# Kernel optimization log

Hardware: AMD Instinct MI355X
Metric: run time of the kernel (lower is better)

## Reference

```python
import jax, jax.numpy as jnp
import numpy as np

DIM = 1024
HEADS = 16
HEAD_DIM = DIM // HEADS
SCALE = HEAD_DIM ** -0.5
B, N = 2, 2048


def setup_inputs() -> dict:
    key = jax.random.key(0)
    ks = jax.random.split(key, 12)
    s = DIM ** -0.5
    return {
        "x_real": jax.random.normal(ks[0], (B, N, DIM), jnp.float32),
        "x_imag": jax.random.normal(ks[1], (B, N, DIM), jnp.float32),
        "Wqkv_r": jax.random.normal(ks[2], (3 * DIM, DIM), jnp.float32) * s,
        "bqkv_r": jax.random.normal(ks[3], (3 * DIM,), jnp.float32) * 0.01,
        "Wqkv_i": jax.random.normal(ks[4], (3 * DIM, DIM), jnp.float32) * s,
        "bqkv_i": jax.random.normal(ks[5], (3 * DIM,), jnp.float32) * 0.01,
        "Wout_r": jax.random.normal(ks[6], (DIM, DIM), jnp.float32) * s,
        "bout_r": jax.random.normal(ks[7], (DIM,), jnp.float32) * 0.01,
        "Wout_i": jax.random.normal(ks[8], (DIM, DIM), jnp.float32) * s,
        "bout_i": jax.random.normal(ks[9], (DIM,), jnp.float32) * 0.01,
    }


def _split_heads(qkv):
    # (B, N, 3*D) -> q, k, v each (B, H, N, hd)
    b, n, _ = qkv.shape
    qkv = qkv.reshape(b, n, 3, HEADS, HEAD_DIM).transpose(2, 0, 3, 1, 4)
    return qkv[0], qkv[1], qkv[2]


def reference(x_real, x_imag, Wqkv_r, bqkv_r, Wqkv_i, bqkv_i,
              Wout_r, bout_r, Wout_i, bout_i):
    b, n, d = x_real.shape
    q_r, k_r, v_r = _split_heads(x_real @ Wqkv_r.T + bqkv_r)
    q_i, k_i, v_i = _split_heads(x_imag @ Wqkv_i.T + bqkv_i)

    # complex score: (q_r + i q_i) (k_r - i k_i)^T pattern per source
    attn_real = (jnp.einsum('bhqd,bhkd->bhqk', q_r, k_r)
                 + jnp.einsum('bhqd,bhkd->bhqk', q_i, k_i)) * SCALE
    attn_imag = (jnp.einsum('bhqd,bhkd->bhqk', q_i, k_r)
                 - jnp.einsum('bhqd,bhkd->bhqk', q_r, k_i)) * SCALE
    attn_mag = jnp.sqrt(attn_real ** 2 + attn_imag ** 2)
    w = jax.nn.softmax(attn_mag, axis=-1)

    out_r = jnp.einsum('bhqk,bhkd->bhqd', w, v_r).transpose(0, 2, 1, 3).reshape(b, n, d)
    out_i = jnp.einsum('bhqk,bhkd->bhqd', w, v_i).transpose(0, 2, 1, 3).reshape(b, n, d)
    out_r = out_r @ Wout_r.T + bout_r
    out_i = out_i @ Wout_i.T + bout_i
    return out_r, out_i
```

## Files before the change

kernel.cpp:

```cpp
#include <hip/hip_runtime.h>


#define DIM_   1024
#define HEADS_ 16
#define HD_    64
#define BB_    2
#define NN_    2048
#define MTOT_  (BB_*NN_)
#define SCALE_ 0.125f
#define QSCALE_ 0.1803368801111243f

typedef __bf16 bf16;
typedef __bf16 bf16x8 __attribute__((ext_vector_type(8)));
typedef short  s16x8  __attribute__((ext_vector_type(8)));
typedef float  fx4    __attribute__((ext_vector_type(4)));

__device__ __forceinline__ bf16x8 neg8(bf16x8 v) {
    s16x8 s;
    __builtin_memcpy(&s, &v, sizeof(s));
    s ^= (short)0x8000;
    bf16x8 r;
    __builtin_memcpy(&r, &s, sizeof(r));
    return r;
}

__device__ __forceinline__ void gl_lds16(const void* g, void* l) {
    __builtin_amdgcn_global_load_lds(
        (const __attribute__((address_space(1))) unsigned int*)g,
        (__attribute__((address_space(3))) unsigned int*)l, 16, 0, 0);
}

#define PIPE_SYNC() asm volatile("s_waitcnt vmcnt(2)\n\ts_barrier" ::: "memory")
#define FULL_SYNC() asm volatile("s_waitcnt vmcnt(0)\n\ts_barrier" ::: "memory")

__global__ __launch_bounds__(256) void cvt_prepass(
    const float* __restrict__ xr, const float* __restrict__ xi,
    const float* __restrict__ wqr, const float* __restrict__ wqi,
    const float* __restrict__ wor, const float* __restrict__ woi,
    bf16* __restrict__ xbf, bf16* __restrict__ wqkv, bf16* __restrict__ wout)
{
    const int bid = blockIdx.x;
    const float* src; bf16* dst; int rel;
    if      (bid < 2048) { src = xr;  dst = xbf;           rel = bid; }
    else if (bid < 4096) { src = xi;  dst = xbf + 4194304; rel = bid - 2048; }
    else if (bid < 5632) { src = wqr; dst = wqkv;          rel = bid - 4096; }
    else if (bid < 7168) { src = wqi; dst = wqkv + 3145728; rel = bid - 5632; }
    else if (bid < 7680) { src = wor; dst = wout;          rel = bid - 7168; }
    else                 { src = woi; dst = wout + 1048576; rel = bid - 7680; }
    size_t base = (size_t)rel * 2048 + (size_t)threadIdx.x * 8;
    fx4 a = *(const fx4*)(src + base);
    fx4 b = *(const fx4*)(src + base + 4);
    bf16x8 o;
#pragma unroll
    for (int j = 0; j < 4; ++j) { o[j] = (bf16)a[j]; o[j+4] = (bf16)b[j]; }
    *(bf16x8*)(dst + base) = o;
}

#define GEMM_CORE(Aptr, Bptr)                                                  \
    __shared__ __align__(16) bf16 As[128*64];                                  \
    __shared__ __align__(16) bf16 Bs[128*64];                                  \
    const int tid  = threadIdx.x;                                              \
    const int w    = tid >> 6, lane = tid & 63;                                \
    const int quad = lane >> 4, lc = lane & 15;                                \
    const int wm   = (w >> 1) * 64, wn = (w & 1) * 64;                         \
    const int rj   = lane >> 3;                                                \
    const int sc   = (lane & 7) ^ rj;                                          \
    const fx4 fzero = {0.f, 0.f, 0.f, 0.f};                                    \
    fx4 acc[4][4];                                                             \
    _Pragma("unroll")                                                          \
    for (int mi = 0; mi < 4; ++mi)                                             \
        _Pragma("unroll")                                                      \
        for (int ni = 0; ni < 4; ++ni) acc[mi][ni] = fzero;                    \
    for (int k0 = 0; k0 < DIM_; k0 += 64) {                                    \
        _Pragma("unroll")                                                      \
        for (int j = 0; j < 4; ++j) {                                          \
            int grp = j*4 + w;                                                 \
            int gr  = grp*8 + rj;                                              \
            gl_lds16(Aptr + (size_t)(m0+gr)*DIM_ + k0 + sc*8, As + grp*512);   \
            gl_lds16(Bptr + (size_t)(n0+gr)*DIM_ + k0 + sc*8, Bs + grp*512);   \
        }                                                                      \
        __syncthreads();                                                       \
        bf16x8 af[2][4], bfr[2][4];                                            \
        _Pragma("unroll")                                                      \
        for (int ks = 0; ks < 2; ++ks) {                                       \
            _Pragma("unroll")                                                  \
            for (int mi = 0; mi < 4; ++mi)                                     \
                af[ks][mi] = *(bf16x8*)&As[(wm+mi*16+lc)*64 + (((ks*4+quad)^(lc&7))*8)]; \
            _Pragma("unroll")                                                  \
            for (int ni = 0; ni < 4; ++ni)                                     \
                bfr[ks][ni] = *(bf16x8*)&Bs[(wn+ni*16+lc)*64 + (((ks*4+quad)^(lc&7))*8)]; \
        }                                                                      \
        _Pragma("unroll")                                                      \
        for (int ks = 0; ks < 2; ++ks)                                         \
            _Pragma("unroll")                                                  \
            for (int mi = 0; mi < 4; ++mi)                                     \
                _Pragma("unroll")                                              \
                for (int ni = 0; ni < 4; ++ni)                                 \
                    acc[mi][ni] = __builtin_amdgcn_mfma_f32_16x16x32_bf16(     \
                        af[ks][mi], bfr[ks][ni], acc[mi][ni], 0, 0, 0);        \
        __syncthreads();                                                       \
    }

__global__ __launch_bounds__(256) void qkv_gemm_dma(
    const bf16* __restrict__ xbf, const bf16* __restrict__ wqkv,
    const float* __restrict__ br, const float* __restrict__ bi,
    bf16* __restrict__ qbuf, bf16* __restrict__ kbuf, bf16* __restrict__ vbuf)
{
    const int z = blockIdx.z;
    const bf16* __restrict__ Ap = xbf  + (size_t)z * 4194304;
    const bf16* __restrict__ Bp = wqkv + (size_t)z * 3145728;
    const float* __restrict__ bias = z ? bi : br;
    const int n0 = blockIdx.x * 128;
    const int m0 = blockIdx.y * 128;

    GEMM_CORE(Ap, Bp)

#pragma unroll
    for (int mi = 0; mi < 4; ++mi)
#pragma unroll
        for (int ni = 0; ni < 4; ++ni)
#pragma unroll
            for (int r = 0; r < 4; ++r) {
                int gm = m0 + wm + mi*16 + quad*4 + r;
                int gc = n0 + wn + ni*16 + lc;
                float val = acc[mi][ni][r] + bias[gc];
                int which = gc >> 10, h = (gc >> 6) & 15, hd = gc & 63;
                if (which == 0) val *= QSCALE_;
                bf16 bv = (bf16)val;
                int b = gm >> 11, n = gm & 2047;
                size_t base = (size_t)((z*BB_ + b)*HEADS_ + h);
                if (which == 0)      qbuf[(base*NN_ + n)*HD_ + hd] = bv;
                else if (which == 1) kbuf[(base*NN_ + n)*HD_ + hd] = bv;
                else                 vbuf[(base*HD_ + hd)*NN_ + n] = bv;
            }
}

__global__ __launch_bounds__(256) void out_gemm_dma(
    const bf16* __restrict__ obuf, const bf16* __restrict__ wout,
    const float* __restrict__ br, const float* __restrict__ bi,
    float* __restrict__ out)
{
    const int z = blockIdx.z;
    const bf16* __restrict__ Ap = obuf + (size_t)z * 4194304;
    const bf16* __restrict__ Bp = wout + (size_t)z * 1048576;
    const float* __restrict__ bias = z ? bi : br;
    float* __restrict__ dst = out + (size_t)z * 4194304;
    const int n0 = blockIdx.x * 128;
    const int m0 = blockIdx.y * 128;

    GEMM_CORE(Ap, Bp)

#pragma unroll
    for (int mi = 0; mi < 4; ++mi)
#pragma unroll
        for (int ni = 0; ni < 4; ++ni)
#pragma unroll
            for (int r = 0; r < 4; ++r) {
                int gm = m0 + wm + mi*16 + quad*4 + r;
                int gc = n0 + wn + ni*16 + lc;
                dst[(size_t)gm*DIM_ + gc] = acc[mi][ni][r] + bias[gc];
            }
}

#define KT 32
#define NSTEP (NN_/KT)

__global__ __launch_bounds__(512, 4) void attn_fwd(
    const bf16* __restrict__ qbuf, const bf16* __restrict__ kbuf,
    const bf16* __restrict__ vbuf, bf16* __restrict__ obuf)
{
    const int bid = blockIdx.x;
    const int xcd = bid & 7;
    const int loc = bid >> 3;
    const int hb  = xcd*4 + (loc >> 4);
    const int blk = loc & 15;
    const int b = hb >> 4, h = hb & 15;

    const int tid  = threadIdx.x;
    const int w    = tid >> 6, lane = tid & 63;
    const int quad = lane >> 4, lc = lane & 15;
    const int q0   = blk*128 + w*16;

    __shared__ __align__(16) bf16 KV[3*8192];

    const size_t hR = (size_t)(b)*HEADS_ + h;
    const size_t hI = (size_t)(BB_ + b)*HEADS_ + h;
    const bf16* qrg = qbuf + hR*NN_*HD_;
    const bf16* qig = qbuf + hI*NN_*HD_;
    const char* krg = (const char*)(kbuf + hR*NN_*HD_);
    const char* kig = (const char*)(kbuf + hI*NN_*HD_);
    const char* vrg = (const char*)(vbuf + hR*HD_*NN_);
    const char* vig = (const char*)(vbuf + hI*HD_*NN_);

    const bf16* pr = qrg + (size_t)(q0 + lc)*HD_ + quad*8;
    const bf16* pi = qig + (size_t)(q0 + lc)*HD_ + quad*8;
    bf16x8 qr0 = *(const bf16x8*)(pr);
    bf16x8 qr1 = *(const bf16x8*)(pr + 32);
    bf16x8 qi0 = *(const bf16x8*)(pi);
    bf16x8 qi1 = *(const bf16x8*)(pi + 32);
    bf16x8 nqr0 = neg8(qr0), nqr1 = neg8(qr1);

    bf16x8 ones;
#pragma unroll
    for (int j = 0; j < 8; ++j) ones[j] = (bf16)1.0f;

    const int arr = w >> 1, half = w & 1;
    const char* stg_base = (arr == 0) ? krg : (arr == 1) ? kig
                         : (arr == 2) ? vrg : vig;
    size_t lane_off, step_mul, j_mul;
    if (arr < 2) {
        const int rl = lane >> 3;
        const int p0 = (rl >> 2)*8 + half*4 + (rl & 3);
        lane_off = (size_t)p0*128 + (size_t)((lane & 7) ^ rl)*16;
        step_mul = 4096;  j_mul = 2048;
    } else {
        lane_off = (size_t)half*131072
                 + (size_t)(lane >> 2)*4096 + (size_t)((lane & 3) ^ ((lane >> 3) & 3))*16;
        step_mul = 64;    j_mul = 65536;
    }
    const char* stg0 = stg_base + lane_off;
    const int lds_base = arr*2048 + half*1024;

    int koff[2][2], voff[4];
#pragma unroll
    for (int kb = 0; kb < 2; ++kb)
#pragma unroll
        for (int hf = 0; hf < 2; ++hf) {
            int r = kb*16 + lc;
            koff[kb][hf] = r*64 + (((hf*4 + quad) ^ (r & 7))*8);
        }
#pragma unroll
    for (int vb = 0; vb < 4; ++vb) {
        int r = vb*16 + lc;
        voff[vb] = r*32 + ((quad ^ ((r >> 1) & 3))*8);
    }

    const fx4 fzero = {0.f, 0.f, 0.f, 0.f};
    fx4 O[2][4];
    fx4 lacc = fzero;
#pragma unroll
    for (int ri = 0; ri < 2; ++ri)
#pragma unroll
        for (int vb = 0; vb < 4; ++vb) O[ri][vb] = fzero;
    bf16x8 pf = {};
    bf16x8 vf[2][4];

    {
        bf16* l = KV + lds_base;
        gl_lds16(stg0,          l);
        gl_lds16(stg0 + j_mul,  l + 512);
        l = KV + 8192 + lds_base;
        gl_lds16(stg0 + step_mul,         l);
        gl_lds16(stg0 + step_mul + j_mul, l + 512);
    }
    PIPE_SYNC();

    int b0 = 0, b1 = 8192, b2 = 16384;
    for (int s = 0; s < NSTEP; ++s) {
        if (s < NSTEP-2) {
            const char* g = stg0 + (size_t)(s+2)*step_mul;
            bf16* l = KV + b2 + lds_base;
            gl_lds16(g,         l);
            gl_lds16(g + j_mul, l + 512);
        }

        if (s > 0) {
            __builtin_amdgcn_s_setprio(1);
#pragma unroll
            for (int ri = 0; ri < 2; ++ri)
#pragma unroll
                for (int vb = 0; vb < 4; ++vb)
                    O[ri][vb] = __builtin_amdgcn_mfma_f32_16x16x32_bf16(
                        pf, vf[ri][vb], O[ri][vb], 0, 0, 0);
            __builtin_amdgcn_s_setprio(0);
        }

        bf16x8 kr_[2][2], ki_[2][2];
#pragma unroll
        for (int kb = 0; kb < 2; ++kb)
#pragma unroll
            for (int hf = 0; hf < 2; ++hf) {
                kr_[kb][hf] = *(bf16x8*)&KV[b0 + koff[kb][hf]];
                ki_[kb][hf] = *(bf16x8*)&KV[b0 + 2048 + koff[kb][hf]];
            }

        fx4 sr[2], si[2];
        __builtin_amdgcn_s_setprio(1);
#pragma unroll
        for (int kb = 0; kb < 2; ++kb) {
            sr[kb] = fzero; si[kb] = fzero;
            sr[kb] = __builtin_amdgcn_mfma_f32_16x16x32_bf16(kr_[kb][0], qr0,  sr[kb], 0,0,0);
            sr[kb] = __builtin_amdgcn_mfma_f32_16x16x32_bf16(kr_[kb][1], qr1,  sr[kb], 0,0,0);
            sr[kb] = __builtin_amdgcn_mfma_f32_16x16x32_bf16(ki_[kb][0], qi0,  sr[kb], 0,0,0);
            sr[kb] = __builtin_amdgcn_mfma_f32_16x16x32_bf16(ki_[kb][1], qi1,  sr[kb], 0,0,0);
            si[kb] = __builtin_amdgcn_mfma_f32_16x16x32_bf16(kr_[kb][0], qi0,  si[kb], 0,0,0);
            si[kb] = __builtin_amdgcn_mfma_f32_16x16x32_bf16(kr_[kb][1], qi1,  si[kb], 0,0,0);
            si[kb] = __builtin_amdgcn_mfma_f32_16x16x32_bf16(ki_[kb][0], nqr0, si[kb], 0,0,0);
            si[kb] = __builtin_amdgcn_mfma_f32_16x16x32_bf16(ki_[kb][1], nqr1, si[kb], 0,0,0);
        }
        __builtin_amdgcn_s_setprio(0);

        float pv8[8];
#pragma unroll
        for (int kb = 0; kb < 2; ++kb)
#pragma unroll
            for (int r4 = 0; r4 < 4; ++r4) {
                float s2 = sr[kb][r4]*sr[kb][r4] + si[kb][r4]*si[kb][r4];
                float mg = __builtin_amdgcn_sqrtf(s2);
                pv8[kb*4 + r4] = __builtin_amdgcn_exp2f(mg);
            }
#pragma unroll
        for (int j = 0; j < 8; ++j) pf[j] = (bf16)pv8[j];

        lacc = __builtin_amdgcn_mfma_f32_16x16x32_bf16(pf, ones, lacc, 0, 0, 0);

#pragma unroll
        for (int ri = 0; ri < 2; ++ri)
#pragma unroll
            for (int vb = 0; vb < 4; ++vb)
                vf[ri][vb] = *(bf16x8*)&KV[b0 + (2+ri)*2048 + voff[vb]];

        if (s == NSTEP-2) FULL_SYNC();
        else              PIPE_SYNC();
        int t = b0; b0 = b1; b1 = b2; b2 = t;
    }

    __builtin_amdgcn_s_setprio(1);
#pragma unroll
    for (int ri = 0; ri < 2; ++ri)
#pragma unroll
        for (int vb = 0; vb < 4; ++vb)
            O[ri][vb] = __builtin_amdgcn_mfma_f32_16x16x32_bf16(
                pf, vf[ri][vb], O[ri][vb], 0, 0, 0);
    __builtin_amdgcn_s_setprio(0);

    float inv[4];
#pragma unroll
    for (int r = 0; r < 4; ++r) inv[r] = 1.f / lacc[r];

    bf16* obr = obuf + ((size_t)(b)*NN_)*DIM_;
    bf16* obi = obuf + ((size_t)(BB_ + b)*NN_)*DIM_;
#pragma unroll
    for (int vb = 0; vb < 4; ++vb)
#pragma unroll
        for (int r = 0; r < 4; ++r) {
            int gn = q0 + quad*4 + r;
            int gc = h*HD_ + vb*16 + lc;
            obr[(size_t)gn*DIM_ + gc] = (bf16)(O[0][vb][r] * inv[r]);
            obi[(size_t)gn*DIM_ + gc] = (bf16)(O[1][vb][r] * inv[r]);
        }
}

__global__ __launch_bounds__(256) void qkv_gemm_legacy(
    const float* __restrict__ xr, const float* __restrict__ xi,
    const float* __restrict__ Wr, const float* __restrict__ Wi,
    const float* __restrict__ br, const float* __restrict__ bi,
    bf16* __restrict__ qbuf, bf16* __restrict__ kbuf, bf16* __restrict__ vbuf)
{
    const int z = blockIdx.z;
    const float* __restrict__ A    = z ? xi : xr;
    const float* __restrict__ W    = z ? Wi : Wr;
    const float* __restrict__ bias = z ? bi : br;
    const int n0 = blockIdx.x * 128;
    const int m0 = blockIdx.y * 128;

    __shared__ bf16 As[128*40];
    __shared__ bf16 Bs[128*40];

    const int tid  = threadIdx.x;
    const int w    = tid >> 6, lane = tid & 63;
    const int quad = lane >> 4, lc = lane & 15;
    const int wm   = (w >> 1) * 64, wn = (w & 1) * 64;

    const fx4 fzero = {0.f, 0.f, 0.f, 0.f};
    fx4 acc[4][4];
#pragma unroll
    for (int mi = 0; mi < 4; ++mi)
#pragma unroll
        for (int ni = 0; ni < 4; ++ni) acc[mi][ni] = fzero;

    for (int k0 = 0; k0 < DIM_; k0 += 32) {
#pragma unroll
        for (int it = 0; it < 2; ++it) {
            int flat = it*2048 + tid*8;
            int row = flat >> 5, col = flat & 31;
            const float* pa = A + (size_t)(m0+row)*DIM_ + k0 + col;
            const float* pb = W + (size_t)(n0+row)*DIM_ + k0 + col;
            fx4 a0 = *(const fx4*)pa, a1 = *(const fx4*)(pa+4);
            fx4 b0 = *(const fx4*)pb, b1 = *(const fx4*)(pb+4);
            bf16x8 av, bv;
#pragma unroll
            for (int j = 0; j < 4; ++j) {
                av[j] = (bf16)a0[j]; av[j+4] = (bf16)a1[j];
                bv[j] = (bf16)b0[j]; bv[j+4] = (bf16)b1[j];
            }
            *(bf16x8*)&As[row*40 + col] = av;
            *(bf16x8*)&Bs[row*40 + col] = bv;
        }
        __syncthreads();

        bf16x8 af[4], bfr[4];
#pragma unroll
        for (int mi = 0; mi < 4; ++mi) af[mi]  = *(bf16x8*)&As[(wm + mi*16 + lc)*40 + quad*8];
#pragma unroll
        for (int ni = 0; ni < 4; ++ni) bfr[ni] = *(bf16x8*)&Bs[(wn + ni*16 + lc)*40 + quad*8];
#pragma unroll
        for (int mi = 0; mi < 4; ++mi)
#pragma unroll
            for (int ni = 0; ni < 4; ++ni)
                acc[mi][ni] = __builtin_amdgcn_mfma_f32_16x16x32_bf16(af[mi], bfr[ni], acc[mi][ni], 0, 0, 0);
        __syncthreads();
    }

#pragma unroll
    for (int mi = 0; mi < 4; ++mi)
#pragma unroll
        for (int ni = 0; ni < 4; ++ni)
#pragma unroll
            for (int r = 0; r < 4; ++r) {
                int gm = m0 + wm + mi*16 + quad*4 + r;
                int gc = n0 + wn + ni*16 + lc;
                float val = acc[mi][ni][r] + bias[gc];
                int which = gc >> 10, h = (gc >> 6) & 15, hd = gc & 63;
                if (which == 0) val *= QSCALE_;
                bf16 bv = (bf16)val;
                int b = gm >> 11, n = gm & 2047;
                size_t base = (size_t)((z*BB_ + b)*HEADS_ + h);
                if (which == 0)      qbuf[(base*NN_ + n)*HD_ + hd] = bv;
                else if (which == 1) kbuf[(base*NN_ + n)*HD_ + hd] = bv;
                else                 vbuf[(base*HD_ + hd)*NN_ + n] = bv;
            }
}

__global__ __launch_bounds__(256) void out_gemm_legacy(
    const bf16* __restrict__ obuf,
    const float* __restrict__ Wr, const float* __restrict__ Wi,
    const float* __restrict__ br, const float* __restrict__ bi,
    float* __restrict__ out)
{
    const int z = blockIdx.z;
    const bf16*  __restrict__ A    = obuf + (size_t)z * MTOT_ * DIM_;
    const float* __restrict__ W    = z ? Wi : Wr;
    const float* __restrict__ bias = z ? bi : br;
    float* __restrict__ dst        = out + (size_t)z * MTOT_ * DIM_;
    const int n0 = blockIdx.x * 128;
    const int m0 = blockIdx.y * 128;

    __shared__ bf16 As[128*40];
    __shared__ bf16 Bs[128*40];

    const int tid  = threadIdx.x;
    const int w    = tid >> 6, lane = tid & 63;
    const int quad = lane >> 4, lc = lane & 15;
    const int wm   = (w >> 1) * 64, wn = (w & 1) * 64;

    const fx4 fzero = {0.f, 0.f, 0.f, 0.f};
    fx4 acc[4][4];
#pragma unroll
    for (int mi = 0; mi < 4; ++mi)
#pragma unroll
        for (int ni = 0; ni < 4; ++ni) acc[mi][ni] = fzero;

    for (int k0 = 0; k0 < DIM_; k0 += 32) {
#pragma unroll
        for (int it = 0; it < 2; ++it) {
            int flat = it*2048 + tid*8;
            int row = flat >> 5, col = flat & 31;
            *(bf16x8*)&As[row*40 + col] = *(const bf16x8*)(A + (size_t)(m0+row)*DIM_ + k0 + col);
            const float* pb = W + (size_t)(n0+row)*DIM_ + k0 + col;
            fx4 b0 = *(const fx4*)pb, b1 = *(const fx4*)(pb+4);
            bf16x8 bv;
#pragma unroll
            for (int j = 0; j < 4; ++j) { bv[j] = (bf16)b0[j]; bv[j+4] = (bf16)b1[j]; }
            *(bf16x8*)&Bs[row*40 + col] = bv;
        }
        __syncthreads();

        bf16x8 af[4], bfr[4];
#pragma unroll
        for (int mi = 0; mi < 4; ++mi) af[mi]  = *(bf16x8*)&As[(wm + mi*16 + lc)*40 + quad*8];
#pragma unroll
        for (int ni = 0; ni < 4; ++ni) bfr[ni] = *(bf16x8*)&Bs[(wn + ni*16 + lc)*40 + quad*8];
#pragma unroll
        for (int mi = 0; mi < 4; ++mi)
#pragma unroll
            for (int ni = 0; ni < 4; ++ni)
                acc[mi][ni] = __builtin_amdgcn_mfma_f32_16x16x32_bf16(af[mi], bfr[ni], acc[mi][ni], 0, 0, 0);
        __syncthreads();
    }

#pragma unroll
    for (int mi = 0; mi < 4; ++mi)
#pragma unroll
        for (int ni = 0; ni < 4; ++ni)
#pragma unroll
            for (int r = 0; r < 4; ++r) {
                int gm = m0 + wm + mi*16 + quad*4 + r;
                int gc = n0 + wn + ni*16 + lc;
                dst[(size_t)gm*DIM_ + gc] = acc[mi][ni][r] + bias[gc];
            }
}

extern "C" void kernel_launch(void* const* d_in, const int* in_sizes, int n_in,
                              void* d_out, int out_size, void* d_ws, size_t ws_size,
                              hipStream_t stream) {
    const float* xr  = (const float*)d_in[0];
    const float* xi  = (const float*)d_in[1];
    const float* Wqr = (const float*)d_in[2];
    const float* bqr = (const float*)d_in[3];
    const float* Wqi = (const float*)d_in[4];
    const float* bqi = (const float*)d_in[5];
    const float* Wor = (const float*)d_in[6];
    const float* bor = (const float*)d_in[7];
    const float* Woi = (const float*)d_in[8];
    const float* boi = (const float*)d_in[9];
    float* out = (float*)d_out;

    bf16* ws = (bf16*)d_ws;
    const size_t NEED = 83886080ull;

    if (ws_size >= NEED) {
        bf16* xbf  = ws;
        bf16* wqkv = ws + 8388608;
        bf16* wout = ws + 14680064;
        bf16* qb   = ws + 16777216;
        bf16* kb   = ws + 25165824;
        bf16* vb   = ws + 33554432;
        bf16* obuf = xbf;

        cvt_prepass<<<dim3(8192), 256, 0, stream>>>(xr, xi, Wqr, Wqi, Wor, Woi,
                                                    xbf, wqkv, wout);
        qkv_gemm_dma<<<dim3(24, 32, 2), 256, 0, stream>>>(xbf, wqkv, bqr, bqi,
                                                          qb, kb, vb);
        attn_fwd<<<dim3(512), 512, 0, stream>>>(qb, kb, vb, obuf);
        out_gemm_dma<<<dim3(8, 32, 2), 256, 0, stream>>>(obuf, wout, bor, boi, out);
    } else {
        const size_t per = (size_t)2 * BB_ * HEADS_ * NN_ * HD_;
        bf16* qb   = ws;
        bf16* kb   = ws + per;
        bf16* vb   = ws + 2*per;
        bf16* obuf = ws + 3*per;
        qkv_gemm_legacy<<<dim3(24, 32, 2), 256, 0, stream>>>(xr, xi, Wqr, Wqi,
                                                             bqr, bqi, qb, kb, vb);
        attn_fwd<<<dim3(512), 512, 0, stream>>>(qb, kb, vb, obuf);
        out_gemm_legacy<<<dim3(8, 32, 2), 256, 0, stream>>>(obuf, Wor, Woi,
                                                            bor, boi, out);
    }
}
```

Before: 337.0 us.

## Triple-buffer GEMM LDS staging with async prefetch and XCD-aware block remap

Replaces the single-buffered GEMM core, which synced twice per 64-wide k-step, with a three-stage ring of 32-wide k tiles. Global-to-LDS DMA loads are issued two stages ahead, and a partial vmcnt wait plus barrier is used instead of a full syncthreads. Block indices are remapped so consecutive tiles spread across XCDs, LDS uses a new XOR swizzle for the 32-column tile, and launch bounds request 3 blocks per CU. The aim is to hide global load latency behind MFMA work in both projection GEMMs. The cost is more LDS per block and extra register pressure.

```diff
diff --git a/kernel.cpp b/kernel.cpp
--- a/kernel.cpp
+++ b/kernel.cpp
@@ -31,6 +31,7 @@
 }
 
 #define PIPE_SYNC() asm volatile("s_waitcnt vmcnt(2)\n\ts_barrier" ::: "memory")
+#define PIPE_G()    asm volatile("s_waitcnt vmcnt(4)\n\ts_barrier" ::: "memory")
 #define FULL_SYNC() asm volatile("s_waitcnt vmcnt(0)\n\ts_barrier" ::: "memory")
 
 __global__ __launch_bounds__(256) void cvt_prepass(
@@ -56,52 +57,60 @@
     *(bf16x8*)(dst + base) = o;
 }
 
-#define GEMM_CORE(Aptr, Bptr)                                                  \
-    __shared__ __align__(16) bf16 As[128*64];                                  \
-    __shared__ __align__(16) bf16 Bs[128*64];                                  \
+#define GEMM_CORE_P(Aptr, Bptr, NWGX)                                          \
+    __shared__ __align__(16) bf16 LS[3*8192];                                  \
     const int tid  = threadIdx.x;                                              \
     const int w    = tid >> 6, lane = tid & 63;                                \
     const int quad = lane >> 4, lc = lane & 15;                                \
     const int wm   = (w >> 1) * 64, wn = (w & 1) * 64;                         \
-    const int rj   = lane >> 3;                                                \
-    const int sc   = (lane & 7) ^ rj;                                          \
+    const int rl   = lane >> 2, cl = lane & 3;                                 \
+    const int swc  = cl ^ ((rl & 3) ^ ((rl >> 2) & 3));                        \
+    const int rsw  = (quad ^ ((lc & 3) ^ ((lc >> 2) & 3))) * 8;                \
+    int flat = blockIdx.y * (NWGX) + blockIdx.x;                               \
+    flat = (flat & 7) * (((NWGX) * 32) / 8) + (flat >> 3);                     \
+    const int m0 = (flat / (NWGX)) * 128;                                      \
+    const int n0 = (flat % (NWGX)) * 128;                                      \
     const fx4 fzero = {0.f, 0.f, 0.f, 0.f};                                    \
     fx4 acc[4][4];                                                             \
     _Pragma("unroll")                                                          \
     for (int mi = 0; mi < 4; ++mi)                                             \
         _Pragma("unroll")                                                      \
         for (int ni = 0; ni < 4; ++ni) acc[mi][ni] = fzero;                    \
-    for (int k0 = 0; k0 < DIM_; k0 += 64) {                                    \
-        _Pragma("unroll")                                                      \
-        for (int j = 0; j < 4; ++j) {                                          \
-            int grp = j*4 + w;                                                 \
-            int gr  = grp*8 + rj;                                              \
-            gl_lds16(Aptr + (size_t)(m0+gr)*DIM_ + k0 + sc*8, As + grp*512);   \
-            gl_lds16(Bptr + (size_t)(n0+gr)*DIM_ + k0 + sc*8, Bs + grp*512);   \
-        }                                                                      \
-        __syncthreads();                                                       \
-        bf16x8 af[2][4], bfr[2][4];                                            \
-        _Pragma("unroll")                                                      \
-        for (int ks = 0; ks < 2; ++ks) {                                       \
+    const bf16* aSrc = Aptr + (size_t)(m0 + w*32 + rl)*DIM_ + swc*8;           \
+    const bf16* bSrc = Bptr + (size_t)(n0 + w*32 + rl)*DIM_ + swc*8;           \
+    auto STG = [&](int kk, int bb) {                                           \
+        gl_lds16(aSrc + kk,                  LS + bb + w*1024);                \
+        gl_lds16(aSrc + kk + 16*DIM_,        LS + bb + w*1024 + 512);          \
+        gl_lds16(bSrc + kk,                  LS + bb + 4096 + w*1024);         \
+        gl_lds16(bSrc + kk + 16*DIM_,        LS + bb + 4096 + w*1024 + 512);   \
+    };                                                                         \
+    STG(0, 0);                                                                 \
+    STG(32, 8192);                                                             \
+    PIPE_G();                                                                  \
+    {                                                                          \
+        int b0 = 0, b1 = 8192, b2 = 16384;                                     \
+        for (int s = 0; s < 32; ++s) {                                         \
+            if (s < 30) STG((s + 2) * 32, b2);                                 \
+            bf16x8 af[4], bfr[4];                                              \
             _Pragma("unroll")                                                  \
             for (int mi = 0; mi < 4; ++mi)                                     \
-                af[ks][mi] = *(bf16x8*)&As[(wm+mi*16+lc)*64 + (((ks*4+quad)^(lc&7))*8)]; \
+                af[mi] = *(bf16x8*)&LS[b0 + (wm + mi*16 + lc)*32 + rsw];       \
             _Pragma("unroll")                                                  \
             for (int ni = 0; ni < 4; ++ni)                                     \
-                bfr[ks][ni] = *(bf16x8*)&Bs[(wn+ni*16+lc)*64 + (((ks*4+quad)^(lc&7))*8)]; \
-        }                                                                      \
-        _Pragma("unroll")                                                      \
-        for (int ks = 0; ks < 2; ++ks)                                         \
+                bfr[ni] = *(bf16x8*)&LS[b0 + 4096 + (wn + ni*16 + lc)*32 + rsw]; \
             _Pragma("unroll")                                                  \
             for (int mi = 0; mi < 4; ++mi)                                     \
                 _Pragma("unroll")                                              \
                 for (int ni = 0; ni < 4; ++ni)                                 \
                     acc[mi][ni] = __builtin_amdgcn_mfma_f32_16x16x32_bf16(     \
-                        af[ks][mi], bfr[ks][ni], acc[mi][ni], 0, 0, 0);        \
-        __syncthreads();                                                       \
-    }
-
-__global__ __launch_bounds__(256) void qkv_gemm_dma(
+                        af[mi], bfr[ni], acc[mi][ni], 0, 0, 0);                \
+            if (s == 30) FULL_SYNC();                                          \
+            else         PIPE_G();                                             \
+            int t = b0; b0 = b1; b1 = b2; b2 = t;                              \
+        }                                                                      \
+    }
+
+__global__ __launch_bounds__(256, 3) void qkv_gemm_dma(
     const bf16* __restrict__ xbf, const bf16* __restrict__ wqkv,
     const float* __restrict__ br, const float* __restrict__ bi,
     bf16* __restrict__ qbuf, bf16* __restrict__ kbuf, bf16* __restrict__ vbuf)
@@ -110,10 +119,8 @@
     const bf16* __restrict__ Ap = xbf  + (size_t)z * 4194304;
     const bf16* __restrict__ Bp = wqkv + (size_t)z * 3145728;
     const float* __restrict__ bias = z ? bi : br;
-    const int n0 = blockIdx.x * 128;
-    const int m0 = blockIdx.y * 128;
-
-    GEMM_CORE(Ap, Bp)
+
+    GEMM_CORE_P(Ap, Bp, 24)
 
 #pragma unroll
     for (int mi = 0; mi < 4; ++mi)
@@ -135,7 +142,7 @@
             }
 }
 
-__global__ __launch_bounds__(256) void out_gemm_dma(
+__global__ __launch_bounds__(256, 3) void out_gemm_dma(
     const bf16* __restrict__ obuf, const bf16* __restrict__ wout,
     const float* __restrict__ br, const float* __restrict__ bi,
     float* __restrict__ out)
@@ -145,10 +152,8 @@
     const bf16* __restrict__ Bp = wout + (size_t)z * 1048576;
     const float* __restrict__ bias = z ? bi : br;
     float* __restrict__ dst = out + (size_t)z * 4194304;
-    const int n0 = blockIdx.x * 128;
-    const int m0 = blockIdx.y * 128;
-
-    GEMM_CORE(Ap, Bp)
+
+    GEMM_CORE_P(Ap, Bp, 8)
 
 #pragma unroll
     for (int mi = 0; mi < 4; ++mi)
```

New measurement: 323.0 us, median of 2. -4.2%, faster.
